# Kernel optimization log

Measured on AMD Instinct MI355X. Metric: run time of the kernel, lower is better.

## Reference

```python
import jax, jax.numpy as jnp
import numpy as np

# graph / model dims
N0, N1, N2 = 200000, 50000, 10000   # nodes per sampled layer (src of hop0, src of hop1, targets)
L = 10                               # tokens per node for embedding sum
E0, E1 = 800000, 160000              # edges per hop
V, IN, H, U, LP = 100000, 128, 256, 32, 128  # vocab, in_channels, hidden, unsup_channels, predictor hidden


def _ln(x, g, b, eps=1e-5):
    m = jnp.mean(x, axis=-1, keepdims=True)
    v = jnp.var(x, axis=-1, keepdims=True)
    return (x - m) * jax.lax.rsqrt(v + eps) * g + b


def _lp_edge(e_i, e_j, w1, b1, g, b, w2, b2):
    # LabelPredictor.edge_forward (eval mode: no dropout)
    h = jnp.concatenate([jnp.abs(e_i - e_j), e_i + e_j, e_i * e_j], axis=-1)  # [E, 3U]
    h = jax.nn.relu(_ln(h @ w1.T + b1, g, b))                                  # [E, LP]
    return jax.nn.sigmoid(h @ w2.T + b2)                                       # [E, 1]


def _conv(x_src, x_tgt, src, dst, n_dst, in_c, ll_w, ll_b, lr_w, lp):
    # LAConv.propagate + message, aggr='add', bipartite (x_src, x_tgt)
    xj = x_src[src]                    # gather [E, in_c+U]
    feat_j = xj[:, :in_c]
    un_j = xj[:, in_c:]
    un_i = x_tgt[dst, in_c:]
    A = jax.lax.stop_gradient(_lp_edge(un_i, un_j, *lp))       # [E, 1], frozen predictor
    A_sum = jax.ops.segment_sum(A, dst, num_segments=n_dst)    # softmax-like normalizer
    A = A / A_sum[dst]
    msg = jnp.concatenate([A * feat_j, un_j], axis=-1)         # [E, in_c+U]
    out = jax.ops.segment_sum(msg, dst, num_segments=n_dst)    # scatter-add aggregate
    out_feat = out[:, :in_c] @ ll_w.T + ll_b + x_tgt[:, :in_c] @ lr_w.T
    return jnp.concatenate([out_feat, out[:, in_c:]], axis=-1)


def setup_inputs() -> dict:
    key = jax.random.key(0)
    ks = jax.random.split(key, 24)
    f = lambda k, shape, s=0.02: (jax.random.normal(k, shape, dtype=jnp.float32) * s)
    inp = {
        'x': jax.random.randint(ks[0], (N0, L), 0, V),
        'x_unsup': jax.random.normal(ks[1], (N0, U), dtype=jnp.float32),
        'src0': jax.random.randint(ks[2], (E0,), 0, N0),
        'dst0': jax.random.randint(ks[3], (E0,), 0, N1),
        'src1': jax.random.randint(ks[4], (E1,), 0, N1),
        'dst1': jax.random.randint(ks[5], (E1,), 0, N2),
        'emb_table': f(ks[6], (V, IN), 1.0),
        'ln_g': jnp.ones((IN,), jnp.float32),
        'ln_b': jnp.zeros((IN,), jnp.float32),
        'lp_w1': f(ks[7], (LP, 3 * U), 0.05),
        'lp_b1': jnp.zeros((LP,), jnp.float32),
        'lp_g': jnp.ones((LP,), jnp.float32),
        'lp_bn': jnp.zeros((LP,), jnp.float32),
        'lp_w2': f(ks[8], (1, LP), 0.05),
        'lp_b2': jnp.zeros((1,), jnp.float32),
        'll_w0': f(ks[9], (H, IN)),
        'll_b0': jnp.zeros((H,), jnp.float32),
        'lr_w0': f(ks[10], (H, IN)),
        'll_w1': f(ks[11], (H, H)),
        'll_b1': jnp.zeros((H,), jnp.float32),
        'lr_w1': f(ks[12], (H, H)),
        'out_w': f(ks[13], (1, H)),
        'out_b': jnp.zeros((1,), jnp.float32),
    }
    return inp


def reference(x, x_unsup, src0, dst0, src1, dst1, emb_table, ln_g, ln_b,
              lp_w1, lp_b1, lp_g, lp_bn, lp_w2, lp_b2,
              ll_w0, ll_b0, lr_w0, ll_w1, ll_b1, lr_w1, out_w, out_b):
    lp = (lp_w1, lp_b1, lp_g, lp_bn, lp_w2, lp_b2)
    # embedding with padding_idx=0 (row 0 contributes zero)
    mask = jnp.concatenate([jnp.zeros((1, 1), jnp.float32), jnp.ones((V - 1, 1), jnp.float32)], axis=0)
    table = emb_table * mask
    e = jnp.sum(table[x], axis=1)                 # [N0, IN]
    e = jax.nn.relu(_ln(e, ln_g, ln_b))
    h = jnp.concatenate([e, x_unsup], axis=-1)    # [N0, IN+U]

    # layer 0 (IN -> H)
    h = _conv(h, h[:N1], src0, dst0, N1, IN, ll_w0, ll_b0, lr_w0, lp)
    feat, un = h[:, :H], h[:, H:]
    h = jnp.concatenate([jax.nn.relu(feat), un], axis=-1)  # eval: no dropout

    # layer 1 (H -> H), last layer: no relu
    h = _conv(h, h[:N2], src1, dst1, N2, H, ll_w1, ll_b1, lr_w1, lp)

    return h[:, :H] @ out_w.T + out_b             # [N2, 1]
```

## Files before the change

### kernel.cpp

```cpp
#include <hip/hip_runtime.h>
#include <hip/hip_bf16.h>
#include <math.h>

#define cN0 200000
#define cN1 50000
#define cN2 10000
#define cL  10
#define cE0 800000
#define cE1 160000
#define cV  100000
#define cIN 128
#define cH  256
#define cU  32
#define cLP 128

typedef __attribute__((ext_vector_type(8))) short short8;
typedef __attribute__((ext_vector_type(4))) float floatx4;

__device__ __forceinline__ float wave_sum(float v) {
#pragma unroll
    for (int m = 1; m < 64; m <<= 1) v += __shfl_xor(v, m);
    return v;
}

__device__ __forceinline__ float red16(float v) {
    v += __shfl_xor(v, 1); v += __shfl_xor(v, 2);
    v += __shfl_xor(v, 4); v += __shfl_xor(v, 8);
    return v;
}

__device__ __forceinline__ unsigned short bf16_rne(float f) {
    union { float f; unsigned u; } c; c.f = f;
    unsigned r = (c.u + 0x7FFFu + ((c.u >> 16) & 1u)) >> 16;
    return (unsigned short)r;
}

__device__ __forceinline__ float b2f(unsigned short u) {
    union { unsigned u; float f; } c; c.u = ((unsigned)u) << 16;
    return c.f;
}

__device__ __forceinline__ unsigned pkbf16(float a, float b) {
    union { __hip_bfloat162 h; unsigned u; } c;
    c.h = __float22bfloat162_rn(make_float2(a, b));
    return c.u;
}

__device__ __forceinline__ float2 unpk(unsigned p) {
    union { unsigned u; float f; } lo, hi;
    lo.u = p << 16; hi.u = p & 0xFFFF0000u;
    return make_float2(lo.f, hi.f);
}

__global__ __launch_bounds__(256) void cvt_all_kernel(const float* __restrict__ emb,
                                                      const float* __restrict__ xu,
                                                      ushort* __restrict__ embB,
                                                      ushort* __restrict__ xub)
{
    size_t i = ((size_t)blockIdx.x * 256 + threadIdx.x) * 4;
    const size_t nEmb = (size_t)cV * cIN;
    const float* s;
    ushort* d;
    size_t j;
    if (i < nEmb) { s = emb; d = embB; j = i; }
    else { s = xu; d = xub; j = i - nEmb; if (j >= (size_t)cN0 * cU) return; }
    float4 v = *(const float4*)&s[j];
    unsigned o0 = pkbf16(v.x, v.y), o1 = pkbf16(v.z, v.w);
    *(uint2*)&d[j] = make_uint2(o0, o1);
}

__global__ __launch_bounds__(256) void cvt_w0_kernel(const float* __restrict__ llw0,
                                                     const float* __restrict__ lrw0,
                                                     ushort* __restrict__ Wb)
{
    int idx = blockIdx.x * 256 + threadIdx.x;
    int i = idx * 2;
    int o = i >> 8, k = i & 255;
    float2 v = (k < 128) ? *(const float2*)&llw0[o * 128 + k]
                         : *(const float2*)&lrw0[o * 128 + (k - 128)];
    *(unsigned*)&Wb[i] = pkbf16(v.x, v.y);
}

__global__ __launch_bounds__(256) void embed_kernel(
    const int* __restrict__ x, const ushort* __restrict__ embB,
    const float* __restrict__ g, const float* __restrict__ b,
    ushort* __restrict__ e0)
{
    int wave = threadIdx.x >> 6, lane = threadIdx.x & 63;
    int n = blockIdx.x * 4 + wave;
    const int* xr = x + (size_t)n * cL;
    int toks[cL];
#pragma unroll
    for (int t = 0; t < cL; ++t) toks[t] = xr[t];
    unsigned packed[cL];
#pragma unroll
    for (int t = 0; t < cL; ++t)
        packed[t] = *(const unsigned*)&embB[(size_t)toks[t] * cIN + 2 * lane];
    float ax = 0.f, ay = 0.f;
#pragma unroll
    for (int t = 0; t < cL; ++t) {
        unsigned p = (toks[t] != 0) ? packed[t] : 0u;
        float2 uv = unpk(p);
        ax += uv.x; ay += uv.y;
    }
    float s1 = wave_sum(ax + ay);
    float s2 = wave_sum(ax * ax + ay * ay);
    float mean = s1 * (1.f / cIN);
    float var = s2 * (1.f / cIN) - mean * mean;
    float rstd = rsqrtf(var + 1e-5f);
    float2 gv = *(const float2*)&g[2 * lane];
    float2 bv = *(const float2*)&b[2 * lane];
    float ox = fmaxf((ax - mean) * rstd * gv.x + bv.x, 0.f);
    float oy = fmaxf((ay - mean) * rstd * gv.y + bv.y, 0.f);
    *(unsigned*)&e0[(size_t)n * cIN + 2 * lane] = pkbf16(ox, oy);
}

__global__ void count_kernel(const int* __restrict__ dst0, const int* __restrict__ dst1,
                             int* __restrict__ cnt0, int* __restrict__ cnt1)
{
    int e = blockIdx.x * 256 + threadIdx.x;
    if (e < cE0) {
        atomicAdd(&cnt0[dst0[e]], 1);
    } else {
        int e1 = e - cE0;
        if (e1 < cE1) atomicAdd(&cnt1[dst1[e1]], 1);
    }
}

__global__ __launch_bounds__(1024) void scan_kernel(const int* __restrict__ cnt0,
                                                    int* __restrict__ off0,
                                                    const int* __restrict__ cnt1,
                                                    int* __restrict__ off1)
{
    const int* cnt = blockIdx.x ? cnt1 : cnt0;
    int* off = blockIdx.x ? off1 : off0;
    int n = blockIdx.x ? cN2 : cN1;
    __shared__ int ps[1024];
    __shared__ int carrySh;
    int t = threadIdx.x;
    if (t == 0) carrySh = 0;
    __syncthreads();
    int ntile = (n + 16383) >> 14;
    for (int tl = 0; tl < ntile; ++tl) {
        int i0 = (tl << 14) + t * 16;
        int v[16];
        if (i0 + 16 <= n) {
            int4 a = *(const int4*)&cnt[i0];
            int4 bq = *(const int4*)&cnt[i0 + 4];
            int4 c = *(const int4*)&cnt[i0 + 8];
            int4 d = *(const int4*)&cnt[i0 + 12];
            v[0] = a.x; v[1] = a.y; v[2] = a.z; v[3] = a.w;
            v[4] = bq.x; v[5] = bq.y; v[6] = bq.z; v[7] = bq.w;
            v[8] = c.x; v[9] = c.y; v[10] = c.z; v[11] = c.w;
            v[12] = d.x; v[13] = d.y; v[14] = d.z; v[15] = d.w;
        } else {
#pragma unroll
            for (int k = 0; k < 16; ++k) v[k] = (i0 + k < n) ? cnt[i0 + k] : 0;
        }
        int s = 0;
#pragma unroll
        for (int k = 0; k < 16; ++k) s += v[k];
        ps[t] = s;
        __syncthreads();
        for (int d = 1; d < 1024; d <<= 1) {
            int x = (t >= d) ? ps[t - d] : 0;
            __syncthreads();
            ps[t] += x;
            __syncthreads();
        }
        int run = ps[t] - s + carrySh;
        if (i0 + 16 <= n) {
            int w[16];
#pragma unroll
            for (int k = 0; k < 16; ++k) { w[k] = run; run += v[k]; }
            *(int4*)&off[i0]      = make_int4(w[0], w[1], w[2], w[3]);
            *(int4*)&off[i0 + 4]  = make_int4(w[4], w[5], w[6], w[7]);
            *(int4*)&off[i0 + 8]  = make_int4(w[8], w[9], w[10], w[11]);
            *(int4*)&off[i0 + 12] = make_int4(w[12], w[13], w[14], w[15]);
        } else {
#pragma unroll
            for (int k = 0; k < 16; ++k)
                if (i0 + k < n) { off[i0 + k] = run; run += v[k]; }
        }
        __syncthreads();
        if (t == 1023) carrySh += ps[1023];
        __syncthreads();
    }
    if (t == 0) off[n] = carrySh;
}

__global__ void scatter_kernel(const int* __restrict__ dst0, const int* __restrict__ dst1,
                               const int* __restrict__ off0, const int* __restrict__ off1,
                               int* __restrict__ pos0, int* __restrict__ pos1,
                               int* __restrict__ eid0, int* __restrict__ eid1)
{
    int e = blockIdx.x * 256 + threadIdx.x;
    if (e < cE0) {
        int d = dst0[e];
        int p = atomicAdd(&pos0[d], 1);
        eid0[off0[d] + p] = e;
    } else {
        int e1 = e - cE0;
        if (e1 < cE1) {
            int d = dst1[e1];
            int p = atomicAdd(&pos1[d], 1);
            eid1[off1[d] + p] = e1;
        }
    }
}

__global__ __launch_bounds__(256) void edge_mlp_mfma_kernel(
    const ushort* __restrict__ uni, int stride_i,
    const ushort* __restrict__ unj, int stride_j,
    const int* __restrict__ src, const int* __restrict__ dst, int E,
    const float* __restrict__ w1, const float* __restrict__ b1v,
    const float* __restrict__ gv, const float* __restrict__ bnv,
    const float* __restrict__ w2, const float* __restrict__ b2,
    float* __restrict__ A)
{
    __shared__ ushort WtL[24 * 512];
    __shared__ float par[cLP * 4];
    int tid = threadIdx.x;
    int lane = tid & 63;
    int n = lane & 15, q = lane >> 4;
    if (tid < cLP) {
        par[tid * 4 + 0] = b1v[tid];
        par[tid * 4 + 1] = gv[tid];
        par[tid * 4 + 2] = bnv[tid];
        par[tid * 4 + 3] = w2[tid];
    }
    if (tid < 64) {
#pragma unroll
        for (int nt = 0; nt < 8; ++nt) {
#pragma unroll
            for (int c = 0; c < 3; ++c) {
                const float* p = &w1[(size_t)(16 * nt + n) * 96 + 32 * c + 8 * q];
                float4 v0 = *(const float4*)p;
                float4 v1 = *(const float4*)(p + 4);
                unsigned* dstw = (unsigned*)&WtL[(nt * 3 + c) * 512 + lane * 8];
                dstw[0] = pkbf16(v0.x, v0.y);
                dstw[1] = pkbf16(v0.z, v0.w);
                dstw[2] = pkbf16(v1.x, v1.y);
                dstw[3] = pkbf16(v1.z, v1.w);
            }
        }
    }
    __syncthreads();
    float b2s = b2[0];

    int wid = blockIdx.x * 4 + (tid >> 6);
    int nw = gridDim.x * 4;
    int ngroups = E >> 4;

    int g = wid;
    uint4 iv = {0, 0, 0, 0}, jv = {0, 0, 0, 0};
    if (g < ngroups) {
        int e = (g << 4) + n;
        int di = dst[e], si = src[e];
        iv = *(const uint4*)&uni[(size_t)di * stride_i + 8 * q];
        jv = *(const uint4*)&unj[(size_t)si * stride_j + 8 * q];
    }
    while (g < ngroups) {
        int gn = g + nw;
        int din = 0, sin = 0;
        if (gn < ngroups) {
            int e2 = (gn << 4) + n;
            din = dst[e2]; sin = src[e2];
        }
        union { short8 s; unsigned u[4]; } a0, a1, a2;
        {
            unsigned iw[4] = {iv.x, iv.y, iv.z, iv.w};
            unsigned jw[4] = {jv.x, jv.y, jv.z, jv.w};
#pragma unroll
            for (int d = 0; d < 4; ++d) {
                float2 u = unpk(iw[d]);
                float2 v = unpk(jw[d]);
                a0.u[d] = pkbf16(fabsf(u.x - v.x), fabsf(u.y - v.y));
                a1.u[d] = pkbf16(u.x + v.x, u.y + v.y);
                a2.u[d] = pkbf16(u.x * v.x, u.y * v.y);
            }
        }
        if (gn < ngroups) {
            iv = *(const uint4*)&uni[(size_t)din * stride_i + 8 * q];
            jv = *(const uint4*)&unj[(size_t)sin * stride_j + 8 * q];
        }
        floatx4 acc[8];
#pragma unroll
        for (int nt = 0; nt < 8; ++nt) acc[nt] = (floatx4){0.f, 0.f, 0.f, 0.f};
#pragma unroll
        for (int nt = 0; nt < 8; ++nt) {
            short8 b0 = *(const short8*)&WtL[(nt * 3 + 0) * 512 + lane * 8];
            short8 b1 = *(const short8*)&WtL[(nt * 3 + 1) * 512 + lane * 8];
            short8 b2w = *(const short8*)&WtL[(nt * 3 + 2) * 512 + lane * 8];
            acc[nt] = __builtin_amdgcn_mfma_f32_16x16x32_bf16(a0.s, b0, acc[nt], 0, 0, 0);
            acc[nt] = __builtin_amdgcn_mfma_f32_16x16x32_bf16(a1.s, b1, acc[nt], 0, 0, 0);
            acc[nt] = __builtin_amdgcn_mfma_f32_16x16x32_bf16(a2.s, b2w, acc[nt], 0, 0, 0);
        }
        float s1[4] = {0.f, 0.f, 0.f, 0.f}, s2[4] = {0.f, 0.f, 0.f, 0.f};
#pragma unroll
        for (int nt = 0; nt < 8; ++nt) {
            float4 pp = *(const float4*)&par[(16 * nt + n) * 4];
#pragma unroll
            for (int r = 0; r < 4; ++r) {
                float h = acc[nt][r] + pp.x;
                acc[nt][r] = h;
                s1[r] += h; s2[r] = fmaf(h, h, s2[r]);
            }
        }
        float rstd[4], mrr[4];
#pragma unroll
        for (int r = 0; r < 4; ++r) {
            s1[r] = red16(s1[r]); s2[r] = red16(s2[r]);
            float mean = s1[r] * (1.f / 128.f);
            float var = s2[r] * (1.f / 128.f) - mean * mean;
            rstd[r] = rsqrtf(var + 1e-5f);
            mrr[r] = mean * rstd[r];
        }
        float p[4] = {0.f, 0.f, 0.f, 0.f};
#pragma unroll
        for (int nt = 0; nt < 8; ++nt) {
            float4 pp = *(const float4*)&par[(16 * nt + n) * 4];
#pragma unroll
            for (int r = 0; r < 4; ++r) {
                float z = fmaf(acc[nt][r], rstd[r], -mrr[r]);
                float y = fmaxf(fmaf(z, pp.y, pp.z), 0.f);
                p[r] = fmaf(y, pp.w, p[r]);
            }
        }
#pragma unroll
        for (int r = 0; r < 4; ++r) p[r] = red16(p[r]);
        if (n < 4) {
            float pv = p[n];
            A[(g << 4) + 4 * q + n] = 1.f / (1.f + expf(-(pv + b2s)));
        }
        g = gn;
    }
}

__global__ __launch_bounds__(256) void agg0_kernel(
    const int* __restrict__ off, const int* __restrict__ eid,
    const int* __restrict__ src, const float* __restrict__ A,
    const ushort* __restrict__ e0, const ushort* __restrict__ xub,
    ushort* __restrict__ aggn, ushort* __restrict__ h1b)
{
    int wave = threadIdx.x >> 6, lane = threadIdx.x & 63;
    int i = blockIdx.x * 4 + wave;
    if (i >= cN1) return;
    int s0 = off[i], s1 = off[i + 1];
    bool feat = lane < 32;
    int col = feat ? (4 * lane) : (4 * (lane & 7));
    const ushort* base = feat ? e0 : xub;
    int stride = feat ? cIN : cU;
    float ax = 0.f, ay = 0.f, az = 0.f, aw = 0.f, accA = 0.f;
    int idx = s0;
    for (; idx + 8 <= s1; idx += 8) {
        int ee[8]; float av[8]; int ss[8]; ushort4 vv[8];
#pragma unroll
        for (int t = 0; t < 8; ++t) ee[t] = eid[idx + t];
#pragma unroll
        for (int t = 0; t < 8; ++t) { av[t] = A[ee[t]]; ss[t] = src[ee[t]]; }
#pragma unroll
        for (int t = 0; t < 8; ++t) vv[t] = *(const ushort4*)&base[(size_t)ss[t] * stride + col];
#pragma unroll
        for (int t = 0; t < 8; ++t) {
            float w = feat ? av[t] : 1.f;
            ax = fmaf(w, b2f(vv[t].x), ax); ay = fmaf(w, b2f(vv[t].y), ay);
            az = fmaf(w, b2f(vv[t].z), az); aw = fmaf(w, b2f(vv[t].w), aw);
            accA += av[t];
        }
    }
    for (; idx + 4 <= s1; idx += 4) {
        int ee[4]; float av[4]; int ss[4]; ushort4 vv[4];
#pragma unroll
        for (int t = 0; t < 4; ++t) ee[t] = eid[idx + t];
#pragma unroll
        for (int t = 0; t < 4; ++t) { av[t] = A[ee[t]]; ss[t] = src[ee[t]]; }
#pragma unroll
        for (int t = 0; t < 4; ++t) vv[t] = *(const ushort4*)&base[(size_t)ss[t] * stride + col];
#pragma unroll
        for (int t = 0; t < 4; ++t) {
            float w = feat ? av[t] : 1.f;
            ax = fmaf(w, b2f(vv[t].x), ax); ay = fmaf(w, b2f(vv[t].y), ay);
            az = fmaf(w, b2f(vv[t].z), az); aw = fmaf(w, b2f(vv[t].w), aw);
            accA += av[t];
        }
    }
    for (; idx < s1; ++idx) {
        int e = eid[idx];
        float a = A[e];
        int s = src[e];
        ushort4 v = *(const ushort4*)&base[(size_t)s * stride + col];
        float w = feat ? a : 1.f;
        ax = fmaf(w, b2f(v.x), ax); ay = fmaf(w, b2f(v.y), ay);
        az = fmaf(w, b2f(v.z), az); aw = fmaf(w, b2f(v.w), aw);
        accA += a;
    }
    if (feat) {
        float r = (accA > 0.f) ? (1.f / accA) : 0.f;
        unsigned o0 = pkbf16(ax * r, ay * r), o1 = pkbf16(az * r, aw * r);
        *(uint2*)&aggn[(size_t)i * cIN + col] = make_uint2(o0, o1);
    } else if (lane < 40) {
        unsigned o0 = pkbf16(ax, ay), o1 = pkbf16(az, aw);
        *(uint2*)&h1b[(size_t)i * 288 + 256 + col] = make_uint2(o0, o1);
    }
}

__global__ __launch_bounds__(256) void linear0_mfma_kernel(
    const ushort* __restrict__ aggn, const ushort* __restrict__ e0,
    const ushort* __restrict__ Wb, const float* __restrict__ bias,
    ushort* __restrict__ h1b)
{
    int tid = threadIdx.x;
    int w = tid >> 6, lane = tid & 63;
    int n = lane & 15, q = lane >> 4;
    short8 Bf[4][8];
    float bia[4];
#pragma unroll
    for (int t = 0; t < 4; ++t) {
        int col = 64 * w + 16 * t + n;
        bia[t] = bias[col];
#pragma unroll
        for (int kc = 0; kc < 8; ++kc)
            Bf[t][kc] = *(const short8*)&Wb[(size_t)col * 256 + kc * 32 + 8 * q];
    }
    for (int g = blockIdx.x; g < cN1 / 16; g += gridDim.x) {
        int m0 = g * 16;
        int row = m0 + n;
        short8 Af[8];
#pragma unroll
        for (int kc = 0; kc < 4; ++kc)
            Af[kc] = *(const short8*)&aggn[(size_t)row * cIN + kc * 32 + 8 * q];
#pragma unroll
        for (int kc = 0; kc < 4; ++kc)
            Af[4 + kc] = *(const short8*)&e0[(size_t)row * cIN + kc * 32 + 8 * q];
#pragma unroll
        for (int t = 0; t < 4; ++t) {
            floatx4 acc = {0.f, 0.f, 0.f, 0.f};
#pragma unroll
            for (int kc = 0; kc < 8; ++kc)
                acc = __builtin_amdgcn_mfma_f32_16x16x32_bf16(Af[kc], Bf[t][kc], acc, 0, 0, 0);
            int col = 64 * w + 16 * t + n;
#pragma unroll
            for (int r = 0; r < 4; ++r) {
                int m = m0 + 4 * q + r;
                h1b[(size_t)m * 288 + col] = bf16_rne(fmaxf(acc[r] + bia[t], 0.f));
            }
        }
    }
}

__global__ __launch_bounds__(256) void precompute_kernel(
    const float* __restrict__ ow, const float* __restrict__ llw1,
    const float* __restrict__ lrw1, const float* __restrict__ llb1,
    const float* __restrict__ ob,
    float* __restrict__ v1, float* __restrict__ v2, float* __restrict__ cbuf)
{
    int b = blockIdx.x;
    int wave = threadIdx.x >> 6, lane = threadIdx.x & 63;
    if (b < 64) {
        int t = b * 4 + wave;
        float s1 = 0.f, s2 = 0.f;
#pragma unroll
        for (int k = 0; k < 4; ++k) {
            int o = lane + 64 * k;
            float wo = ow[o];
            s1 = fmaf(wo, llw1[o * 256 + t], s1);
            s2 = fmaf(wo, lrw1[o * 256 + t], s2);
        }
        s1 = wave_sum(s1); s2 = wave_sum(s2);
        if (lane == 0) { v1[t] = s1; v2[t] = s2; }
    } else if (wave == 0) {
        float s = 0.f;
#pragma unroll
        for (int k = 0; k < 4; ++k) {
            int t = lane + 64 * k;
            s = fmaf(ow[t], llb1[t], s);
        }
        s = wave_sum(s);
        if (lane == 0) cbuf[0] = s + ob[0];
    }
}

__global__ __launch_bounds__(256) void agg1_final_kernel(
    const int* __restrict__ off, const int* __restrict__ eid,
    const int* __restrict__ src, const float* __restrict__ A,
    const ushort* __restrict__ h1b, const float* __restrict__ v1,
    const float* __restrict__ v2, const float* __restrict__ cbuf,
    float* __restrict__ out)
{
    int wave = threadIdx.x >> 6, lane = threadIdx.x & 63;
    int n = blockIdx.x * 4 + wave;
    if (n >= cN2) return;
    int s0 = off[n], s1 = off[n + 1];
    float ax = 0.f, ay = 0.f, az = 0.f, aw = 0.f, accA = 0.f;
    int idx = s0;
    for (; idx + 8 <= s1; idx += 8) {
        int ee[8]; float av[8]; int ss[8]; ushort4 vv[8];
#pragma unroll
        for (int t = 0; t < 8; ++t) ee[t] = eid[idx + t];
#pragma unroll
        for (int t = 0; t < 8; ++t) { av[t] = A[ee[t]]; ss[t] = src[ee[t]]; }
#pragma unroll
        for (int t = 0; t < 8; ++t) vv[t] = *(const ushort4*)&h1b[(size_t)ss[t] * 288 + 4 * lane];
#pragma unroll
        for (int t = 0; t < 8; ++t) {
            ax = fmaf(av[t], b2f(vv[t].x), ax); ay = fmaf(av[t], b2f(vv[t].y), ay);
            az = fmaf(av[t], b2f(vv[t].z), az); aw = fmaf(av[t], b2f(vv[t].w), aw);
            accA += av[t];
        }
    }
    for (; idx + 4 <= s1; idx += 4) {
        int ee[4]; float av[4]; int ss[4]; ushort4 vv[4];
#pragma unroll
        for (int t = 0; t < 4; ++t) ee[t] = eid[idx + t];
#pragma unroll
        for (int t = 0; t < 4; ++t) { av[t] = A[ee[t]]; ss[t] = src[ee[t]]; }
#pragma unroll
        for (int t = 0; t < 4; ++t) vv[t] = *(const ushort4*)&h1b[(size_t)ss[t] * 288 + 4 * lane];
#pragma unroll
        for (int t = 0; t < 4; ++t) {
            ax = fmaf(av[t], b2f(vv[t].x), ax); ay = fmaf(av[t], b2f(vv[t].y), ay);
            az = fmaf(av[t], b2f(vv[t].z), az); aw = fmaf(av[t], b2f(vv[t].w), aw);
            accA += av[t];
        }
    }
    for (; idx < s1; ++idx) {
        int e = eid[idx];
        float a = A[e];
        int s = src[e];
        ushort4 v = *(const ushort4*)&h1b[(size_t)s * 288 + 4 * lane];
        ax = fmaf(a, b2f(v.x), ax); ay = fmaf(a, b2f(v.y), ay);
        az = fmaf(a, b2f(v.z), az); aw = fmaf(a, b2f(v.w), aw);
        accA += a;
    }
    float r = (accA > 0.f) ? (1.f / accA) : 0.f;
    ushort4 t4 = *(const ushort4*)&h1b[(size_t)n * 288 + 4 * lane];
    float4 w1v = *(const float4*)&v1[4 * lane];
    float4 w2v = *(const float4*)&v2[4 * lane];
    float p = r * (ax * w1v.x + ay * w1v.y + az * w1v.z + aw * w1v.w)
            + b2f(t4.x) * w2v.x + b2f(t4.y) * w2v.y
            + b2f(t4.z) * w2v.z + b2f(t4.w) * w2v.w;
    p = wave_sum(p);
    if (lane == 0) out[n] = p + cbuf[0];
}

extern "C" void kernel_launch(void* const* d_in, const int* in_sizes, int n_in,
                              void* d_out, int out_size, void* d_ws, size_t ws_size,
                              hipStream_t stream)
{
    const int*   x     = (const int*)d_in[0];
    const float* xu    = (const float*)d_in[1];
    const int*   src0  = (const int*)d_in[2];
    const int*   dst0  = (const int*)d_in[3];
    const int*   src1  = (const int*)d_in[4];
    const int*   dst1  = (const int*)d_in[5];
    const float* emb   = (const float*)d_in[6];
    const float* ln_g  = (const float*)d_in[7];
    const float* ln_b  = (const float*)d_in[8];
    const float* lp_w1 = (const float*)d_in[9];
    const float* lp_b1 = (const float*)d_in[10];
    const float* lp_g  = (const float*)d_in[11];
    const float* lp_bn = (const float*)d_in[12];
    const float* lp_w2 = (const float*)d_in[13];
    const float* lp_b2 = (const float*)d_in[14];
    const float* ll_w0 = (const float*)d_in[15];
    const float* ll_b0 = (const float*)d_in[16];
    const float* lr_w0 = (const float*)d_in[17];
    const float* ll_w1 = (const float*)d_in[18];
    const float* ll_b1 = (const float*)d_in[19];
    const float* lr_w1 = (const float*)d_in[20];
    const float* out_w = (const float*)d_in[21];
    const float* out_b = (const float*)d_in[22];
    float* out = (float*)d_out;

    char* ws = (char*)d_ws;
    size_t off = 0;
    auto alloc = [&](size_t bytes) -> void* {
        void* p = ws + off;
        off = (off + bytes + 255) & ~(size_t)255;
        return p;
    };
    ushort* embB = (ushort*)alloc((size_t)cV * cIN * 2);
    ushort* xub  = (ushort*)alloc((size_t)cN0 * cU * 2);
    ushort* e0   = (ushort*)alloc((size_t)cN0 * cIN * 2);
    ushort* aggn = (ushort*)alloc((size_t)cN1 * cIN * 2);
    ushort* h1b  = (ushort*)alloc((size_t)cN1 * 288 * 2);
    float* A0    = (float*)alloc((size_t)cE0 * 4);
    float* A1    = (float*)alloc((size_t)cE1 * 4);
    ushort* Wb   = (ushort*)alloc((size_t)256 * 256 * 2);
    float* v1    = (float*)alloc(256 * 4);
    float* v2    = (float*)alloc(256 * 4);
    float* cbuf  = (float*)alloc(64);
    char* zbase  = ws + off;
    int* cnt0    = (int*)alloc((size_t)cN1 * 4);
    int* pos0    = (int*)alloc((size_t)cN1 * 4);
    int* cnt1    = (int*)alloc((size_t)cN2 * 4);
    int* pos1    = (int*)alloc((size_t)cN2 * 4);
    size_t zlen  = (size_t)((ws + off) - zbase);
    int* off0    = (int*)alloc((size_t)(cN1 + 1) * 4);
    int* off1    = (int*)alloc((size_t)(cN2 + 1) * 4);
    int* eid0    = (int*)alloc((size_t)cE0 * 4);
    int* eid1    = (int*)alloc((size_t)cE1 * 4);

    hipMemsetAsync(zbase, 0, zlen, stream);

    cvt_all_kernel<<<(cV * cIN + cN0 * cU) / 1024, 256, 0, stream>>>(emb, xu, embB, xub);
    cvt_w0_kernel<<<128, 256, 0, stream>>>(ll_w0, lr_w0, Wb);
    precompute_kernel<<<65, 256, 0, stream>>>(out_w, ll_w1, lr_w1, ll_b1, out_b, v1, v2, cbuf);

    embed_kernel<<<cN0 / 4, 256, 0, stream>>>(x, embB, ln_g, ln_b, e0);

    count_kernel<<<(cE0 + cE1 + 255) / 256, 256, 0, stream>>>(dst0, dst1, cnt0, cnt1);
    scan_kernel<<<2, 1024, 0, stream>>>(cnt0, off0, cnt1, off1);
    scatter_kernel<<<(cE0 + cE1 + 255) / 256, 256, 0, stream>>>(dst0, dst1, off0, off1,
                                                                pos0, pos1, eid0, eid1);

    edge_mlp_mfma_kernel<<<1024, 256, 0, stream>>>(xub, cU, xub, cU, src0, dst0, cE0,
                                                   lp_w1, lp_b1, lp_g, lp_bn, lp_w2, lp_b2, A0);

    agg0_kernel<<<(cN1 + 3) / 4, 256, 0, stream>>>(off0, eid0, src0, A0, e0, xub, aggn, h1b);

    linear0_mfma_kernel<<<784, 256, 0, stream>>>(aggn, e0, Wb, ll_b0, h1b);

    edge_mlp_mfma_kernel<<<512, 256, 0, stream>>>(h1b + 256, 288, h1b + 256, 288, src1, dst1, cE1,
                                                  lp_w1, lp_b1, lp_g, lp_bn, lp_w2, lp_b2, A1);

    agg1_final_kernel<<<(cN2 + 3) / 4, 256, 0, stream>>>(off1, eid1, src1, A1, h1b, v1, v2, cbuf, out);
}
```

Before: 556.7 us.

## Fuse independent stages into combined prep, mid and tail kernels

Independent kernels are merged into three horizontally fused launches. Weight/table conversion, edge counting and precompute become one prep kernel. The layer-0 edge MLP is interleaved with edge scatter and embedding, and the layer-1 edge MLP is interleaved with the linear0 MFMA. The goal is to cut launch overhead and let memory-bound and compute-bound work share the GPU at the same time. The risk is that every block in the fused kernels statically reserves the edge-MLP shared memory, which can lower occupancy for the lightweight scatter, embed and linear blocks.

```diff
diff --git a/kernel.cpp b/kernel.cpp
--- a/kernel.cpp
+++ b/kernel.cpp
@@ -14,6 +14,14 @@
 #define cU  32
 #define cLP 128
 
+#define PREP_CVT   18750
+#define PREP_CNT   22500
+#define PREP_W0    22628
+#define PREP_TOT   22693
+#define MID_MAIN   54272
+#define MID_TOT    54774
+#define TAIL_TOT   1296
+
 typedef __attribute__((ext_vector_type(8))) short short8;
 typedef __attribute__((ext_vector_type(4))) float floatx4;
 
@@ -52,78 +60,185 @@
     return make_float2(lo.f, hi.f);
 }
 
-__global__ __launch_bounds__(256) void cvt_all_kernel(const float* __restrict__ emb,
-                                                      const float* __restrict__ xu,
-                                                      ushort* __restrict__ embB,
-                                                      ushort* __restrict__ xub)
-{
-    size_t i = ((size_t)blockIdx.x * 256 + threadIdx.x) * 4;
-    const size_t nEmb = (size_t)cV * cIN;
-    const float* s;
-    ushort* d;
-    size_t j;
-    if (i < nEmb) { s = emb; d = embB; j = i; }
-    else { s = xu; d = xub; j = i - nEmb; if (j >= (size_t)cN0 * cU) return; }
-    float4 v = *(const float4*)&s[j];
-    unsigned o0 = pkbf16(v.x, v.y), o1 = pkbf16(v.z, v.w);
-    *(uint2*)&d[j] = make_uint2(o0, o1);
-}
-
-__global__ __launch_bounds__(256) void cvt_w0_kernel(const float* __restrict__ llw0,
-                                                     const float* __restrict__ lrw0,
-                                                     ushort* __restrict__ Wb)
-{
-    int idx = blockIdx.x * 256 + threadIdx.x;
-    int i = idx * 2;
-    int o = i >> 8, k = i & 255;
-    float2 v = (k < 128) ? *(const float2*)&llw0[o * 128 + k]
-                         : *(const float2*)&lrw0[o * 128 + (k - 128)];
-    *(unsigned*)&Wb[i] = pkbf16(v.x, v.y);
-}
-
-__global__ __launch_bounds__(256) void embed_kernel(
-    const int* __restrict__ x, const ushort* __restrict__ embB,
-    const float* __restrict__ g, const float* __restrict__ b,
-    ushort* __restrict__ e0)
-{
-    int wave = threadIdx.x >> 6, lane = threadIdx.x & 63;
-    int n = blockIdx.x * 4 + wave;
-    const int* xr = x + (size_t)n * cL;
-    int toks[cL];
-#pragma unroll
-    for (int t = 0; t < cL; ++t) toks[t] = xr[t];
-    unsigned packed[cL];
-#pragma unroll
-    for (int t = 0; t < cL; ++t)
-        packed[t] = *(const unsigned*)&embB[(size_t)toks[t] * cIN + 2 * lane];
-    float ax = 0.f, ay = 0.f;
-#pragma unroll
-    for (int t = 0; t < cL; ++t) {
-        unsigned p = (toks[t] != 0) ? packed[t] : 0u;
-        float2 uv = unpk(p);
-        ax += uv.x; ay += uv.y;
-    }
-    float s1 = wave_sum(ax + ay);
-    float s2 = wave_sum(ax * ax + ay * ay);
-    float mean = s1 * (1.f / cIN);
-    float var = s2 * (1.f / cIN) - mean * mean;
-    float rstd = rsqrtf(var + 1e-5f);
-    float2 gv = *(const float2*)&g[2 * lane];
-    float2 bv = *(const float2*)&b[2 * lane];
-    float ox = fmaxf((ax - mean) * rstd * gv.x + bv.x, 0.f);
-    float oy = fmaxf((ay - mean) * rstd * gv.y + bv.y, 0.f);
-    *(unsigned*)&e0[(size_t)n * cIN + 2 * lane] = pkbf16(ox, oy);
-}
-
-__global__ void count_kernel(const int* __restrict__ dst0, const int* __restrict__ dst1,
-                             int* __restrict__ cnt0, int* __restrict__ cnt1)
-{
-    int e = blockIdx.x * 256 + threadIdx.x;
-    if (e < cE0) {
-        atomicAdd(&cnt0[dst0[e]], 1);
+__device__ __forceinline__ void edge_mlp_body(
+    ushort* WtL, float* par, int tid,
+    const ushort* __restrict__ uni, int stride_i,
+    const ushort* __restrict__ unj, int stride_j,
+    const int* __restrict__ src, const int* __restrict__ dst, int E,
+    const float* __restrict__ w1, const float* __restrict__ b1v,
+    const float* __restrict__ gv, const float* __restrict__ bnv,
+    const float* __restrict__ w2, const float* __restrict__ b2,
+    float* __restrict__ A, int wid, int nw)
+{
+    int lane = tid & 63;
+    int n = lane & 15, q = lane >> 4;
+    if (tid < cLP) {
+        par[tid * 4 + 0] = b1v[tid];
+        par[tid * 4 + 1] = gv[tid];
+        par[tid * 4 + 2] = bnv[tid];
+        par[tid * 4 + 3] = w2[tid];
+    }
+    if (tid < 64) {
+#pragma unroll
+        for (int nt = 0; nt < 8; ++nt) {
+#pragma unroll
+            for (int c = 0; c < 3; ++c) {
+                const float* p = &w1[(size_t)(16 * nt + n) * 96 + 32 * c + 8 * q];
+                float4 v0 = *(const float4*)p;
+                float4 v1 = *(const float4*)(p + 4);
+                unsigned* dstw = (unsigned*)&WtL[(nt * 3 + c) * 512 + lane * 8];
+                dstw[0] = pkbf16(v0.x, v0.y);
+                dstw[1] = pkbf16(v0.z, v0.w);
+                dstw[2] = pkbf16(v1.x, v1.y);
+                dstw[3] = pkbf16(v1.z, v1.w);
+            }
+        }
+    }
+    __syncthreads();
+    float b2s = b2[0];
+    int ngroups = E >> 4;
+    int g = wid;
+    uint4 iv = {0, 0, 0, 0}, jv = {0, 0, 0, 0};
+    if (g < ngroups) {
+        int e = (g << 4) + n;
+        int di = dst[e], si = src[e];
+        iv = *(const uint4*)&uni[(size_t)di * stride_i + 8 * q];
+        jv = *(const uint4*)&unj[(size_t)si * stride_j + 8 * q];
+    }
+    while (g < ngroups) {
+        int gn = g + nw;
+        int din = 0, sin = 0;
+        if (gn < ngroups) {
+            int e2 = (gn << 4) + n;
+            din = dst[e2]; sin = src[e2];
+        }
+        union { short8 s; unsigned u[4]; } a0, a1, a2;
+        {
+            unsigned iw[4] = {iv.x, iv.y, iv.z, iv.w};
+            unsigned jw[4] = {jv.x, jv.y, jv.z, jv.w};
+#pragma unroll
+            for (int d = 0; d < 4; ++d) {
+                float2 u = unpk(iw[d]);
+                float2 v = unpk(jw[d]);
+                a0.u[d] = pkbf16(fabsf(u.x - v.x), fabsf(u.y - v.y));
+                a1.u[d] = pkbf16(u.x + v.x, u.y + v.y);
+                a2.u[d] = pkbf16(u.x * v.x, u.y * v.y);
+            }
+        }
+        if (gn < ngroups) {
+            iv = *(const uint4*)&uni[(size_t)din * stride_i + 8 * q];
+            jv = *(const uint4*)&unj[(size_t)sin * stride_j + 8 * q];
+        }
+        floatx4 acc[8];
+#pragma unroll
+        for (int nt = 0; nt < 8; ++nt) acc[nt] = (floatx4){0.f, 0.f, 0.f, 0.f};
+#pragma unroll
+        for (int nt = 0; nt < 8; ++nt) {
+            short8 b0 = *(const short8*)&WtL[(nt * 3 + 0) * 512 + lane * 8];
+            short8 b1 = *(const short8*)&WtL[(nt * 3 + 1) * 512 + lane * 8];
+            short8 b2w = *(const short8*)&WtL[(nt * 3 + 2) * 512 + lane * 8];
+            acc[nt] = __builtin_amdgcn_mfma_f32_16x16x32_bf16(a0.s, b0, acc[nt], 0, 0, 0);
+            acc[nt] = __builtin_amdgcn_mfma_f32_16x16x32_bf16(a1.s, b1, acc[nt], 0, 0, 0);
+            acc[nt] = __builtin_amdgcn_mfma_f32_16x16x32_bf16(a2.s, b2w, acc[nt], 0, 0, 0);
+        }
+        float s1[4] = {0.f, 0.f, 0.f, 0.f}, s2[4] = {0.f, 0.f, 0.f, 0.f};
+#pragma unroll
+        for (int nt = 0; nt < 8; ++nt) {
+            float4 pp = *(const float4*)&par[(16 * nt + n) * 4];
+#pragma unroll
+            for (int r = 0; r < 4; ++r) {
+                float h = acc[nt][r] + pp.x;
+                acc[nt][r] = h;
+                s1[r] += h; s2[r] = fmaf(h, h, s2[r]);
+            }
+        }
+        float rstd[4], mrr[4];
+#pragma unroll
+        for (int r = 0; r < 4; ++r) {
+            s1[r] = red16(s1[r]); s2[r] = red16(s2[r]);
+            float mean = s1[r] * (1.f / 128.f);
+            float var = s2[r] * (1.f / 128.f) - mean * mean;
+            rstd[r] = rsqrtf(var + 1e-5f);
+            mrr[r] = mean * rstd[r];
+        }
+        float p[4] = {0.f, 0.f, 0.f, 0.f};
+#pragma unroll
+        for (int nt = 0; nt < 8; ++nt) {
+            float4 pp = *(const float4*)&par[(16 * nt + n) * 4];
+#pragma unroll
+            for (int r = 0; r < 4; ++r) {
+                float z = fmaf(acc[nt][r], rstd[r], -mrr[r]);
+                float y = fmaxf(fmaf(z, pp.y, pp.z), 0.f);
+                p[r] = fmaf(y, pp.w, p[r]);
+            }
+        }
+#pragma unroll
+        for (int r = 0; r < 4; ++r) p[r] = red16(p[r]);
+        if (n < 4) {
+            float pv = p[n];
+            A[(g << 4) + 4 * q + n] = 1.f / (1.f + expf(-(pv + b2s)));
+        }
+        g = gn;
+    }
+}
+
+__global__ __launch_bounds__(256) void prep_kernel(
+    const float* __restrict__ emb, const float* __restrict__ xu,
+    ushort* __restrict__ embB, ushort* __restrict__ xub,
+    const int* __restrict__ dst0, const int* __restrict__ dst1,
+    int* __restrict__ cnt0, int* __restrict__ cnt1,
+    const float* __restrict__ llw0, const float* __restrict__ lrw0,
+    ushort* __restrict__ Wb,
+    const float* __restrict__ ow, const float* __restrict__ llw1,
+    const float* __restrict__ lrw1, const float* __restrict__ llb1,
+    const float* __restrict__ ob,
+    float* __restrict__ v1, float* __restrict__ v2, float* __restrict__ cbuf)
+{
+    int b = blockIdx.x;
+    int tid = threadIdx.x;
+    if (b < PREP_CVT) {
+        size_t i = ((size_t)b * 256 + tid) * 4;
+        const size_t nEmb = (size_t)cV * cIN;
+        const float* s; ushort* d; size_t j;
+        if (i < nEmb) { s = emb; d = embB; j = i; }
+        else { s = xu; d = xub; j = i - nEmb; }
+        float4 v = *(const float4*)&s[j];
+        *(uint2*)&d[j] = make_uint2(pkbf16(v.x, v.y), pkbf16(v.z, v.w));
+    } else if (b < PREP_CNT) {
+        int e = (b - PREP_CVT) * 256 + tid;
+        if (e < cE0) atomicAdd(&cnt0[dst0[e]], 1);
+        else atomicAdd(&cnt1[dst1[e - cE0]], 1);
+    } else if (b < PREP_W0) {
+        int i = ((b - PREP_CNT) * 256 + tid) * 2;
+        int o = i >> 8, k = i & 255;
+        float2 v = (k < 128) ? *(const float2*)&llw0[o * 128 + k]
+                             : *(const float2*)&lrw0[o * 128 + (k - 128)];
+        *(unsigned*)&Wb[i] = pkbf16(v.x, v.y);
     } else {
-        int e1 = e - cE0;
-        if (e1 < cE1) atomicAdd(&cnt1[dst1[e1]], 1);
+        int bb = b - PREP_W0;
+        int wave = tid >> 6, lane = tid & 63;
+        if (bb < 64) {
+            int t = bb * 4 + wave;
+            float s1 = 0.f, s2 = 0.f;
+#pragma unroll
+            for (int k = 0; k < 4; ++k) {
+                int o = lane + 64 * k;
+                float wo = ow[o];
+                s1 = fmaf(wo, llw1[o * 256 + t], s1);
+                s2 = fmaf(wo, lrw1[o * 256 + t], s2);
+            }
+            s1 = wave_sum(s1); s2 = wave_sum(s2);
+            if (lane == 0) { v1[t] = s1; v2[t] = s2; }
+        } else if (wave == 0) {
+            float s = 0.f;
+#pragma unroll
+            for (int k = 0; k < 4; ++k) {
+                int t = lane + 64 * k;
+                s = fmaf(ow[t], llb1[t], s);
+            }
+            s = wave_sum(s);
+            if (lane == 0) cbuf[0] = s + ob[0];
+        }
     }
 }
 
@@ -189,151 +304,78 @@
     if (t == 0) off[n] = carrySh;
 }
 
-__global__ void scatter_kernel(const int* __restrict__ dst0, const int* __restrict__ dst1,
-                               const int* __restrict__ off0, const int* __restrict__ off1,
-                               int* __restrict__ pos0, int* __restrict__ pos1,
-                               int* __restrict__ eid0, int* __restrict__ eid1)
-{
-    int e = blockIdx.x * 256 + threadIdx.x;
-    if (e < cE0) {
-        int d = dst0[e];
-        int p = atomicAdd(&pos0[d], 1);
-        eid0[off0[d] + p] = e;
+__global__ __launch_bounds__(256) void mid_kernel(
+    const ushort* __restrict__ xub,
+    const int* __restrict__ src0, const int* __restrict__ dst0,
+    const float* __restrict__ w1, const float* __restrict__ b1v,
+    const float* __restrict__ gv, const float* __restrict__ bnv,
+    const float* __restrict__ w2, const float* __restrict__ b2,
+    float* __restrict__ A0,
+    const int* __restrict__ x, const ushort* __restrict__ embB,
+    const float* __restrict__ g, const float* __restrict__ bvec,
+    ushort* __restrict__ e0,
+    const int* __restrict__ dst1,
+    const int* __restrict__ off0, const int* __restrict__ off1,
+    int* __restrict__ pos0, int* __restrict__ pos1,
+    int* __restrict__ eid0, int* __restrict__ eid1)
+{
+    __shared__ ushort WtL[24 * 512];
+    __shared__ float par[cLP * 4];
+    int b = blockIdx.x;
+    int tid = threadIdx.x;
+    int other_id;
+    if (b < MID_MAIN) {
+        int eb = b / 53;
+        if (b - eb * 53 == 0) {
+            int wid = eb * 4 + (tid >> 6);
+            edge_mlp_body(WtL, par, tid, xub, cU, xub, cU, src0, dst0, cE0,
+                          w1, b1v, gv, bnv, w2, b2, A0, wid, 4096);
+            return;
+        }
+        other_id = b - eb - 1;
     } else {
-        int e1 = e - cE0;
-        if (e1 < cE1) {
+        other_id = 53248 + (b - MID_MAIN);
+    }
+    if (other_id < 3750) {
+        int e = other_id * 256 + tid;
+        if (e < cE0) {
+            int d = dst0[e];
+            int p = atomicAdd(&pos0[d], 1);
+            eid0[off0[d] + p] = e;
+        } else {
+            int e1 = e - cE0;
             int d = dst1[e1];
             int p = atomicAdd(&pos1[d], 1);
             eid1[off1[d] + p] = e1;
         }
-    }
-}
-
-__global__ __launch_bounds__(256) void edge_mlp_mfma_kernel(
-    const ushort* __restrict__ uni, int stride_i,
-    const ushort* __restrict__ unj, int stride_j,
-    const int* __restrict__ src, const int* __restrict__ dst, int E,
-    const float* __restrict__ w1, const float* __restrict__ b1v,
-    const float* __restrict__ gv, const float* __restrict__ bnv,
-    const float* __restrict__ w2, const float* __restrict__ b2,
-    float* __restrict__ A)
-{
-    __shared__ ushort WtL[24 * 512];
-    __shared__ float par[cLP * 4];
-    int tid = threadIdx.x;
-    int lane = tid & 63;
-    int n = lane & 15, q = lane >> 4;
-    if (tid < cLP) {
-        par[tid * 4 + 0] = b1v[tid];
-        par[tid * 4 + 1] = gv[tid];
-        par[tid * 4 + 2] = bnv[tid];
-        par[tid * 4 + 3] = w2[tid];
-    }
-    if (tid < 64) {
-#pragma unroll
-        for (int nt = 0; nt < 8; ++nt) {
-#pragma unroll
-            for (int c = 0; c < 3; ++c) {
-                const float* p = &w1[(size_t)(16 * nt + n) * 96 + 32 * c + 8 * q];
-                float4 v0 = *(const float4*)p;
-                float4 v1 = *(const float4*)(p + 4);
-                unsigned* dstw = (unsigned*)&WtL[(nt * 3 + c) * 512 + lane * 8];
-                dstw[0] = pkbf16(v0.x, v0.y);
-                dstw[1] = pkbf16(v0.z, v0.w);
-                dstw[2] = pkbf16(v1.x, v1.y);
-                dstw[3] = pkbf16(v1.z, v1.w);
-            }
-        }
-    }
-    __syncthreads();
-    float b2s = b2[0];
-
-    int wid = blockIdx.x * 4 + (tid >> 6);
-    int nw = gridDim.x * 4;
-    int ngroups = E >> 4;
-
-    int g = wid;
-    uint4 iv = {0, 0, 0, 0}, jv = {0, 0, 0, 0};
-    if (g < ngroups) {
-        int e = (g << 4) + n;
-        int di = dst[e], si = src[e];
-        iv = *(const uint4*)&uni[(size_t)di * stride_i + 8 * q];
-        jv = *(const uint4*)&unj[(size_t)si * stride_j + 8 * q];
-    }
-    while (g < ngroups) {
-        int gn = g + nw;
-        int din = 0, sin = 0;
-        if (gn < ngroups) {
-            int e2 = (gn << 4) + n;
-            din = dst[e2]; sin = src[e2];
-        }
-        union { short8 s; unsigned u[4]; } a0, a1, a2;
-        {
-            unsigned iw[4] = {iv.x, iv.y, iv.z, iv.w};
-            unsigned jw[4] = {jv.x, jv.y, jv.z, jv.w};
-#pragma unroll
-            for (int d = 0; d < 4; ++d) {
-                float2 u = unpk(iw[d]);
-                float2 v = unpk(jw[d]);
-                a0.u[d] = pkbf16(fabsf(u.x - v.x), fabsf(u.y - v.y));
-                a1.u[d] = pkbf16(u.x + v.x, u.y + v.y);
-                a2.u[d] = pkbf16(u.x * v.x, u.y * v.y);
-            }
-        }
-        if (gn < ngroups) {
-            iv = *(const uint4*)&uni[(size_t)din * stride_i + 8 * q];
-            jv = *(const uint4*)&unj[(size_t)sin * stride_j + 8 * q];
-        }
-        floatx4 acc[8];
-#pragma unroll
-        for (int nt = 0; nt < 8; ++nt) acc[nt] = (floatx4){0.f, 0.f, 0.f, 0.f};
-#pragma unroll
-        for (int nt = 0; nt < 8; ++nt) {
-            short8 b0 = *(const short8*)&WtL[(nt * 3 + 0) * 512 + lane * 8];
-            short8 b1 = *(const short8*)&WtL[(nt * 3 + 1) * 512 + lane * 8];
-            short8 b2w = *(const short8*)&WtL[(nt * 3 + 2) * 512 + lane * 8];
-            acc[nt] = __builtin_amdgcn_mfma_f32_16x16x32_bf16(a0.s, b0, acc[nt], 0, 0, 0);
-            acc[nt] = __builtin_amdgcn_mfma_f32_16x16x32_bf16(a1.s, b1, acc[nt], 0, 0, 0);
-            acc[nt] = __builtin_amdgcn_mfma_f32_16x16x32_bf16(a2.s, b2w, acc[nt], 0, 0, 0);
-        }
-        float s1[4] = {0.f, 0.f, 0.f, 0.f}, s2[4] = {0.f, 0.f, 0.f, 0.f};
-#pragma unroll
-        for (int nt = 0; nt < 8; ++nt) {
-            float4 pp = *(const float4*)&par[(16 * nt + n) * 4];
-#pragma unroll
-            for (int r = 0; r < 4; ++r) {
-                float h = acc[nt][r] + pp.x;
-                acc[nt][r] = h;
-                s1[r] += h; s2[r] = fmaf(h, h, s2[r]);
-            }
-        }
-        float rstd[4], mrr[4];
-#pragma unroll
-        for (int r = 0; r < 4; ++r) {
-            s1[r] = red16(s1[r]); s2[r] = red16(s2[r]);
-            float mean = s1[r] * (1.f / 128.f);
-            float var = s2[r] * (1.f / 128.f) - mean * mean;
-            rstd[r] = rsqrtf(var + 1e-5f);
-            mrr[r] = mean * rstd[r];
-        }
-        float p[4] = {0.f, 0.f, 0.f, 0.f};
-#pragma unroll
-        for (int nt = 0; nt < 8; ++nt) {
-            float4 pp = *(const float4*)&par[(16 * nt + n) * 4];
-#pragma unroll
-            for (int r = 0; r < 4; ++r) {
-                float z = fmaf(acc[nt][r], rstd[r], -mrr[r]);
-                float y = fmaxf(fmaf(z, pp.y, pp.z), 0.f);
-                p[r] = fmaf(y, pp.w, p[r]);
-            }
-        }
-#pragma unroll
-        for (int r = 0; r < 4; ++r) p[r] = red16(p[r]);
-        if (n < 4) {
-            float pv = p[n];
-            A[(g << 4) + 4 * q + n] = 1.f / (1.f + expf(-(pv + b2s)));
-        }
-        g = gn;
+    } else {
+        int wave = tid >> 6, lane = tid & 63;
+        int n = (other_id - 3750) * 4 + wave;
+        const int* xr = x + (size_t)n * cL;
+        int toks[cL];
+#pragma unroll
+        for (int t = 0; t < cL; ++t) toks[t] = xr[t];
+        unsigned packed[cL];
+#pragma unroll
+        for (int t = 0; t < cL; ++t)
+            packed[t] = *(const unsigned*)&embB[(size_t)toks[t] * cIN + 2 * lane];
+        float ax = 0.f, ay = 0.f;
+#pragma unroll
+        for (int t = 0; t < cL; ++t) {
+            unsigned p = (toks[t] != 0) ? packed[t] : 0u;
+            float2 uv = unpk(p);
+            ax += uv.x; ay += uv.y;
+        }
+        float s1 = wave_sum(ax + ay);
+        float s2 = wave_sum(ax * ax + ay * ay);
+        float mean = s1 * (1.f / cIN);
+        float var = s2 * (1.f / cIN) - mean * mean;
+        float rstd = rsqrtf(var + 1e-5f);
+        float2 gv2 = *(const float2*)&g[2 * lane];
+        float2 bv2 = *(const float2*)&bvec[2 * lane];
+        float ox = fmaxf((ax - mean) * rstd * gv2.x + bv2.x, 0.f);
+        float oy = fmaxf((ay - mean) * rstd * gv2.y + bv2.y, 0.f);
+        *(unsigned*)&e0[(size_t)n * cIN + 2 * lane] = pkbf16(ox, oy);
     }
 }
 
@@ -405,12 +447,29 @@
     }
 }
 
-__global__ __launch_bounds__(256) void linear0_mfma_kernel(
+__global__ __launch_bounds__(256) void tail_kernel(
     const ushort* __restrict__ aggn, const ushort* __restrict__ e0,
     const ushort* __restrict__ Wb, const float* __restrict__ bias,
-    ushort* __restrict__ h1b)
-{
+    ushort* __restrict__ h1b,
+    const int* __restrict__ src1, const int* __restrict__ dst1,
+    const float* __restrict__ w1, const float* __restrict__ b1v,
+    const float* __restrict__ gv, const float* __restrict__ bnv,
+    const float* __restrict__ w2, const float* __restrict__ b2,
+    float* __restrict__ A1)
+{
+    __shared__ ushort WtL[24 * 512];
+    __shared__ float par[cLP * 4];
+    int b = blockIdx.x;
     int tid = threadIdx.x;
+    bool isEdge = (b < 1024) && (b & 1);
+    if (isEdge) {
+        int eb = b >> 1;
+        int wid = eb * 4 + (tid >> 6);
+        edge_mlp_body(WtL, par, tid, h1b + 256, 288, h1b + 256, 288, src1, dst1, cE1,
+                      w1, b1v, gv, bnv, w2, b2, A1, wid, 2048);
+        return;
+    }
+    int lb = (b < 1024) ? (b >> 1) : (512 + (b - 1024));
     int w = tid >> 6, lane = tid & 63;
     int n = lane & 15, q = lane >> 4;
     short8 Bf[4][8];
@@ -423,7 +482,7 @@
         for (int kc = 0; kc < 8; ++kc)
             Bf[t][kc] = *(const short8*)&Wb[(size_t)col * 256 + kc * 32 + 8 * q];
     }
-    for (int g = blockIdx.x; g < cN1 / 16; g += gridDim.x) {
+    for (int g = lb; g < cN1 / 16; g += 784) {
         int m0 = g * 16;
         int row = m0 + n;
         short8 Af[8];
@@ -446,38 +505,6 @@
                 h1b[(size_t)m * 288 + col] = bf16_rne(fmaxf(acc[r] + bia[t], 0.f));
             }
         }
-    }
-}
-
-__global__ __launch_bounds__(256) void precompute_kernel(
-    const float* __restrict__ ow, const float* __restrict__ llw1,
-    const float* __restrict__ lrw1, const float* __restrict__ llb1,
-    const float* __restrict__ ob,
-    float* __restrict__ v1, float* __restrict__ v2, float* __restrict__ cbuf)
-{
-    int b = blockIdx.x;
-    int wave = threadIdx.x >> 6, lane = threadIdx.x & 63;
-    if (b < 64) {
-        int t = b * 4 + wave;
-        float s1 = 0.f, s2 = 0.f;
-#pragma unroll
-        for (int k = 0; k < 4; ++k) {
-            int o = lane + 64 * k;
-            float wo = ow[o];
-            s1 = fmaf(wo, llw1[o * 256 + t], s1);
-            s2 = fmaf(wo, lrw1[o * 256 + t], s2);
-        }
-        s1 = wave_sum(s1); s2 = wave_sum(s2);
-        if (lane == 0) { v1[t] = s1; v2[t] = s2; }
-    } else if (wave == 0) {
-        float s = 0.f;
-#pragma unroll
-        for (int k = 0; k < 4; ++k) {
-            int t = lane + 64 * k;
-            s = fmaf(ow[t], llb1[t], s);
-        }
-        s = wave_sum(s);
-        if (lane == 0) cbuf[0] = s + ob[0];
     }
 }
 
@@ -604,26 +631,22 @@
 
     hipMemsetAsync(zbase, 0, zlen, stream);
 
-    cvt_all_kernel<<<(cV * cIN + cN0 * cU) / 1024, 256, 0, stream>>>(emb, xu, embB, xub);
-    cvt_w0_kernel<<<128, 256, 0, stream>>>(ll_w0, lr_w0, Wb);
-    precompute_kernel<<<65, 256, 0, stream>>>(out_w, ll_w1, lr_w1, ll_b1, out_b, v1, v2, cbuf);
-
-    embed_kernel<<<cN0 / 4, 256, 0, stream>>>(x, embB, ln_g, ln_b, e0);
-
-    count_kernel<<<(cE0 + cE1 + 255) / 256, 256, 0, stream>>>(dst0, dst1, cnt0, cnt1);
+    prep_kernel<<<PREP_TOT, 256, 0, stream>>>(emb, xu, embB, xub, dst0, dst1, cnt0, cnt1,
+                                              ll_w0, lr_w0, Wb, out_w, ll_w1, lr_w1,
+                                              ll_b1, out_b, v1, v2, cbuf);
+
     scan_kernel<<<2, 1024, 0, stream>>>(cnt0, off0, cnt1, off1);
-    scatter_kernel<<<(cE0 + cE1 + 255) / 256, 256, 0, stream>>>(dst0, dst1, off0, off1,
-                                                                pos0, pos1, eid0, eid1);
-
-    edge_mlp_mfma_kernel<<<1024, 256, 0, stream>>>(xub, cU, xub, cU, src0, dst0, cE0,
-                                                   lp_w1, lp_b1, lp_g, lp_bn, lp_w2, lp_b2, A0);
+
+    mid_kernel<<<MID_TOT, 256, 0, stream>>>(xub, src0, dst0,
+                                            lp_w1, lp_b1, lp_g, lp_bn, lp_w2, lp_b2, A0,
+                                            x, embB, ln_g, ln_b, e0,
+                                            dst1, off0, off1, pos0, pos1, eid0, eid1);
 
     agg0_kernel<<<(cN1 + 3) / 4, 256, 0, stream>>>(off0, eid0, src0, A0, e0, xub, aggn, h1b);
 
-    linear0_mfma_kernel<<<784, 256, 0, stream>>>(aggn, e0, Wb, ll_b0, h1b);
-
-    edge_mlp_mfma_kernel<<<512, 256, 0, stream>>>(h1b + 256, 288, h1b + 256, 288, src1, dst1, cE1,
-                                                  lp_w1, lp_b1, lp_g, lp_bn, lp_w2, lp_b2, A1);
+    tail_kernel<<<TAIL_TOT, 256, 0, stream>>>(aggn, e0, Wb, ll_b0, h1b,
+                                              src1, dst1,
+                                              lp_w1, lp_b1, lp_g, lp_bn, lp_w2, lp_b2, A1);
 
     agg1_final_kernel<<<(cN2 + 3) / 4, 256, 0, stream>>>(off1, eid1, src1, A1, h1b, v1, v2, cbuf, out);
 }
```

Measured after the change: 638.4 us. 14.7% more time.
